# Performance work log

Hardware: AMD Instinct MI355X
Metric: run time of the kernel (lower is better)

Reference implementation:

```python
import jax, jax.numpy as jnp
import numpy as np

N_NODES = 16384
N_EDGES = 131072
N_GRAPHS = 16
U_SZ, U_RED = 4096, 256
EDGE_H, EDGE_OUT = 1024, 512
NODE_H = 512
NODE_IN = 9  # 4 + 5, hard-coded in OGRENet
EDGE_IN = 1


def _lin_init(k, fan_in, fan_out):
    k1, k2 = jax.random.split(k)
    bound = 1.0 / np.sqrt(fan_in)
    W = jax.random.uniform(k1, (fan_in, fan_out), jnp.float32, -bound, bound)
    b = jax.random.uniform(k2, (fan_out,), jnp.float32, -bound, bound)
    return W, b


def setup_inputs() -> dict:
    key = jax.random.key(0)
    ks = jax.random.split(key, 16)
    inp = {
        "x": jax.random.normal(ks[0], (N_NODES, NODE_IN), jnp.float32),
        "edge_attr": jax.random.normal(ks[1], (N_EDGES, EDGE_IN), jnp.float32),
        "u": jax.random.normal(ks[2], (N_GRAPHS, U_SZ), jnp.float32),
        "edge_index": jax.random.randint(ks[3], (2, N_EDGES), 0, N_NODES, jnp.int64 if jax.config.jax_enable_x64 else jnp.int32).astype(jnp.int32),
        "batch": jnp.sort(jax.random.randint(ks[4], (N_NODES,), 0, N_GRAPHS)).astype(jnp.int32),
    }
    # global dim reduction 4096 -> 256
    inp["w_dr"], inp["b_dr"] = _lin_init(ks[5], U_SZ, U_RED)
    # edge MLP: in = 1 + 2*9 + 256 = 275
    e_in = EDGE_IN + 2 * NODE_IN + U_RED
    inp["e_w0"], inp["e_b0"] = _lin_init(ks[6], e_in, EDGE_H)
    inp["e_w1"], inp["e_b1"] = _lin_init(ks[7], EDGE_H, EDGE_H)
    inp["e_w2"], inp["e_b2"] = _lin_init(ks[8], EDGE_H, EDGE_H)
    inp["e_w3"], inp["e_b3"] = _lin_init(ks[9], EDGE_H, EDGE_H)
    inp["e_wf"], inp["e_bf"] = _lin_init(ks[10], EDGE_H, EDGE_OUT)
    # node mlp 1: in = 9 + 512 = 521
    inp["n1_w0"], inp["n1_b0"] = _lin_init(ks[11], NODE_IN + EDGE_OUT, NODE_H)
    inp["n1_w1"], inp["n1_b1"] = _lin_init(ks[12], NODE_H, NODE_H)
    # node mlp 2: in = 9 + 512 + 256 = 777, out = 1
    inp["n2_w0"], inp["n2_b0"] = _lin_init(ks[13], NODE_IN + NODE_H + U_RED, NODE_H)
    inp["n2_w1"], inp["n2_b1"] = _lin_init(ks[14], NODE_H, 1)
    return inp


def reference(x, edge_attr, u, edge_index, batch,
              w_dr, b_dr,
              e_w0, e_b0, e_w1, e_b1, e_w2, e_b2, e_w3, e_b3, e_wf, e_bf,
              n1_w0, n1_b0, n1_w1, n1_b1,
              n2_w0, n2_b0, n2_w1, n2_b1):
    relu = jax.nn.relu
    # select_dim_reduction
    u_r = u @ w_dr + b_dr  # [G, 256]
    row, col = edge_index[0], edge_index[1]
    # EdgeModel: cat([src, dest, edge_attr, u[batch[row]]])
    e_in = jnp.concatenate([x[row], x[col], edge_attr, u_r[batch[row]]], axis=1)
    h = relu(e_in @ e_w0 + e_b0)
    h = relu(h @ e_w1 + e_b1)
    h = relu(h @ e_w2 + e_b2)
    h = relu(h @ e_w3 + e_b3)
    e = h @ e_wf + e_bf  # [E, 512]
    # NodeModel: mlp1 on cat([x[col], edge_attr_new]) then scatter_mean by row
    n_in = jnp.concatenate([x[col], e], axis=1)
    h = relu(n_in @ n1_w0 + n1_b0)
    h = relu(h @ n1_w1 + n1_b1)  # [E, 512]
    agg = jax.ops.segment_sum(h, row, num_segments=N_NODES)
    cnt = jax.ops.segment_sum(jnp.ones((h.shape[0],), h.dtype), row, num_segments=N_NODES)
    agg = agg / jnp.maximum(cnt, 1.0)[:, None]  # scatter_mean (zeros stay zero)
    o = jnp.concatenate([x, agg, u_r[batch]], axis=1)
    o = relu(o @ n2_w0 + n2_b0) @ n2_w1 + n2_b1  # [N, 1]
    return jnp.squeeze(o, axis=-1)
```

## Files before the change

kernel.cpp:

```cpp
#include <hip/hip_runtime.h>
#include <type_traits>
#include <utility>
#include <cstdint>

typedef unsigned short u16;
typedef __attribute__((ext_vector_type(4))) float f32x4;
typedef __attribute__((ext_vector_type(8))) short s16x8;
typedef __attribute__((ext_vector_type(8))) __bf16 b16x8;

template <typename T, typename = void> struct MfmaTakes : std::false_type {};
template <typename T>
struct MfmaTakes<T, std::void_t<decltype(__builtin_amdgcn_mfma_f32_16x16x32_bf16(
    std::declval<T>(), std::declval<T>(), std::declval<f32x4>(), 0, 0, 0))>>
    : std::true_type {};
using abvec = std::conditional_t<MfmaTakes<s16x8>::value, s16x8, b16x8>;
static_assert(sizeof(abvec) == 16, "frag must be 4 VGPRs");

template <typename T>
__device__ __forceinline__ f32x4 mfma_bf16(T a, T b, f32x4 c) {
  return __builtin_amdgcn_mfma_f32_16x16x32_bf16(a, b, c, 0, 0, 0);
}

__device__ __forceinline__ float b2f(u16 v) {
  union { unsigned u; float f; } x; x.u = ((unsigned)v) << 16; return x.f;
}
__device__ __forceinline__ u16 f2b(float f) {
  union { float f; unsigned u; } x; x.f = f;
  unsigned r = x.u + 0x7fffu + ((x.u >> 16) & 1u);
  return (u16)(r >> 16);
}

__device__ __forceinline__ void gld16(const void* g, void* l) {
  auto gp = reinterpret_cast<const __attribute__((address_space(1))) unsigned int*>(
      reinterpret_cast<uintptr_t>(g));
  auto lp = reinterpret_cast<__attribute__((address_space(3))) unsigned int*>(
      reinterpret_cast<uintptr_t>(l));
  __builtin_amdgcn_global_load_lds(gp, lp, 16, 0, 0);
}

#define NN 16384
#define NE 131072
#define NG 16

__global__ void detect_dtype(const u16* __restrict__ x, int* __restrict__ flag) {
  __shared__ int cnt;
  if (threadIdx.x == 0) cnt = 0;
  __syncthreads();
  int local = 0;
#pragma unroll
  for (int i = 0; i < 8; i++) {
    u16 h = x[threadIdx.x * 8 + i];
    int e = (h >> 7) & 0xFF;
    if (h == 0 || (e >= 110 && e <= 134)) local++;
  }
  atomicAdd(&cnt, local);
  __syncthreads();
  if (threadIdx.x == 0) *flag = (cnt >= 1700) ? 1 : 0;
}

struct CvtJob {
  const void* src[14];
  void* dst[14];
  int n[14];
};

__global__ __launch_bounds__(256) void cvt_all(CvtJob jb, const int* __restrict__ flag) {
  const int idx = blockIdx.x * 256 + threadIdx.x;
  const int f = *flag;
  int off = 0;
#pragma unroll
  for (int j = 0; j < 14; j++) {
    const int nn = jb.n[j];
    if (idx < off + nn) {
      const int i = idx - off;
      u16 v = f ? ((const u16*)jb.src[j])[i]
                : f2b(((const float*)jb.src[j])[i]);
      ((u16*)jb.dst[j])[i] = v;
      return;
    }
    off += nn;
  }
}

__global__ __launch_bounds__(256) void cvt_plain(
    const void* __restrict__ src, u16* __restrict__ dst, int n,
    const int* __restrict__ flag)
{
  const int i = blockIdx.x * 256 + threadIdx.x;
  if (i >= n) return;
  dst[i] = *flag ? ((const u16*)src)[i] : f2b(((const float*)src)[i]);
}

__global__ __launch_bounds__(256, 3) void gemm_bt(
    const u16* __restrict__ A, const u16* __restrict__ Bt,
    const u16* __restrict__ bias, u16* __restrict__ C,
    int M, int N, int K, int ldc, int relu)
{
  __shared__ alignas(16) u16 smem[24576];
  const int tid = threadIdx.x;
  const int wave = tid >> 6, lane = tid & 63;
  const int m0 = blockIdx.x * 128, n0 = blockIdx.y * 128;

  const int srow = lane >> 2;
  const int kslot = lane & 3;
  const int sswz = (srow >> 1) & 3;
  const u16* gA = A + (size_t)(m0 + wave * 32 + srow) * K + (kslot ^ sswz) * 8;
  const u16* gB = Bt + (size_t)(n0 + wave * 32 + srow) * K + (kslot ^ sswz) * 8;
  const int loff = (wave * 32 + srow) * 32 + kslot * 8;

  const int wm = (wave >> 1) * 64;
  const int wn = (wave & 1) * 64;
  const int fr = lane & 15;
  const int fks = ((lane >> 4) ^ ((fr >> 1) & 3)) * 8;

  f32x4 acc[4][4] = {};
  const int NT = K >> 5;

#define STAGE(t, s) do { \
    const int o_ = (t) * 32; \
    u16* S_ = smem + (s) * 8192; \
    gld16(gA + o_, S_ + loff); gld16(gA + 16 * (size_t)K + o_, S_ + loff + 512); \
    gld16(gB + o_, S_ + 4096 + loff); gld16(gB + 16 * (size_t)K + o_, S_ + 4096 + loff + 512); \
  } while (0)

  STAGE(0, 0);
  if (NT > 1) {
    STAGE(1, 1);
    __asm__ volatile("s_waitcnt vmcnt(4)" ::: "memory");
  } else {
    __asm__ volatile("s_waitcnt vmcnt(0)" ::: "memory");
  }
  __builtin_amdgcn_s_barrier();

  int sl = 0;
  for (int t = 0; t < NT; t++) {
    if (t + 2 < NT) {
      const int sw = (sl + 2 >= 3) ? sl - 1 : sl + 2;
      STAGE(t + 2, sw);
    }
    const u16* As = smem + sl * 8192;
    const u16* Bs = As + 4096;
    abvec af[4], bf[4];
#pragma unroll
    for (int i = 0; i < 4; i++)
      af[i] = *(const abvec*)&As[(wm + i * 16 + fr) * 32 + fks];
#pragma unroll
    for (int i = 0; i < 4; i++)
      bf[i] = *(const abvec*)&Bs[(wn + i * 16 + fr) * 32 + fks];
    __builtin_amdgcn_s_setprio(1);
#pragma unroll
    for (int mi = 0; mi < 4; mi++)
#pragma unroll
      for (int ni = 0; ni < 4; ni++)
        acc[mi][ni] = mfma_bf16(af[mi], bf[ni], acc[mi][ni]);
    __builtin_amdgcn_s_setprio(0);
    if (t + 2 < NT) __asm__ volatile("s_waitcnt vmcnt(4)" ::: "memory");
    else            __asm__ volatile("s_waitcnt vmcnt(0)" ::: "memory");
    __builtin_amdgcn_s_barrier();
    sl = (sl == 2) ? 0 : sl + 1;
  }
#undef STAGE

  const int crow0 = (lane >> 4) * 4;
  float bv[4];
#pragma unroll
  for (int ni = 0; ni < 4; ni++) bv[ni] = b2f(bias[n0 + wn + ni * 16 + fr]);

  u16* W = smem + wave * 4096;
#pragma unroll
  for (int mi = 0; mi < 4; mi++) {
#pragma unroll
    for (int ni = 0; ni < 4; ni++) {
      f32x4 v = acc[mi][ni];
      const int colx = ni * 16 + fr;
      const int cl = colx & 7, ch = colx >> 3;
#pragma unroll
      for (int r = 0; r < 4; r++) {
        const int rowx = mi * 16 + crow0 + r;
        float f = v[r] + bv[ni];
        if (relu) f = fmaxf(f, 0.0f);
        W[rowx * 64 + ((ch ^ (rowx & 7)) << 3) + cl] = f2b(f);
      }
    }
  }
  __asm__ volatile("s_waitcnt lgkmcnt(0)" ::: "memory");
#pragma unroll
  for (int p = 0; p < 8; p++) {
    const int rowx = p * 8 + (lane >> 3);
    const int pc = lane & 7;
    const int lc = pc ^ (rowx & 7);
    s16x8 val = *(const s16x8*)&W[rowx * 64 + pc * 8];
    *(s16x8*)&C[(size_t)(m0 + wm + rowx) * ldc + n0 + wn + lc * 8] = val;
  }
}

__global__ __launch_bounds__(1024) void gemm256b(
    const u16* __restrict__ A, const u16* __restrict__ Bt,
    const u16* __restrict__ bias, u16* __restrict__ C,
    int K, int ldc, int relu)
{
  __shared__ alignas(16) u16 smem[49152];
  const int tid = threadIdx.x;
  const int wave = tid >> 6, lane = tid & 63;
  const int wr = wave >> 2, wc = wave & 3;
  const int m0 = blockIdx.x << 8, n0 = blockIdx.y << 8;

  const int srow = tid >> 2;
  const int kslot = tid & 3;
  const int sswz = (srow >> 1) & 3;
  const u16* gA = A  + (size_t)(m0 + srow) * K + (kslot ^ sswz) * 8;
  const u16* gB = Bt + (size_t)(n0 + srow) * K + (kslot ^ sswz) * 8;
  const int loff = tid * 8;

  const int fr = lane & 15;
  const int fks = ((lane >> 4) ^ ((fr >> 1) & 3)) * 8;
  const int aob = (wr * 64 + fr) * 32 + fks;
  const int bob = (wc * 64 + fr) * 32 + fks;

  f32x4 acc[4][4] = {};
  const int NT = K >> 5;

#define STAGE2(t, s) do { \
    const int o_ = (t) * 32; \
    u16* S_ = smem + (s) * 16384; \
    gld16(gA + o_, S_ + loff); gld16(gB + o_, S_ + 8192 + loff); \
  } while (0)

  STAGE2(0, 0);
  if (NT > 1) {
    STAGE2(1, 1);
    __asm__ volatile("s_waitcnt vmcnt(2)" ::: "memory");
  } else {
    __asm__ volatile("s_waitcnt vmcnt(0)" ::: "memory");
  }
  __builtin_amdgcn_s_barrier();

  int sl = 0;
  for (int t = 0; t < NT; t++) {
    if (t + 2 < NT) {
      const int sw = (sl + 2 >= 3) ? sl - 1 : sl + 2;
      STAGE2(t + 2, sw);
    }
    const u16* As = smem + sl * 16384;
    const u16* Bs = As + 8192;
    abvec af[4], bf[4];
#pragma unroll
    for (int i = 0; i < 4; i++)
      af[i] = *(const abvec*)&As[aob + i * 512];
#pragma unroll
    for (int i = 0; i < 4; i++)
      bf[i] = *(const abvec*)&Bs[bob + i * 512];
    __builtin_amdgcn_s_setprio(1);
#pragma unroll
    for (int mi = 0; mi < 4; mi++)
#pragma unroll
      for (int ni = 0; ni < 4; ni++)
        acc[mi][ni] = mfma_bf16(af[mi], bf[ni], acc[mi][ni]);
    __builtin_amdgcn_s_setprio(0);
    if (t + 2 < NT) __asm__ volatile("s_waitcnt vmcnt(2)" ::: "memory");
    else            __asm__ volatile("s_waitcnt vmcnt(0)" ::: "memory");
    __builtin_amdgcn_s_barrier();
    sl = (sl == 2) ? 0 : sl + 1;
  }
#undef STAGE2

  const int crow0 = (lane >> 4) * 4;
  float bv[4];
#pragma unroll
  for (int ni = 0; ni < 4; ni++) bv[ni] = b2f(bias[n0 + wc * 64 + ni * 16 + fr]);
  u16* W = smem + wave * 2048;
#pragma unroll
  for (int h = 0; h < 2; h++) {
    if (h) __asm__ volatile("s_waitcnt lgkmcnt(0)" ::: "memory");
#pragma unroll
    for (int mi = 0; mi < 4; mi++) {
#pragma unroll
      for (int nh = 0; nh < 2; nh++) {
        const int ni = h * 2 + nh;
        f32x4 v = acc[mi][ni];
        const int colx = nh * 16 + fr;
        const int cl = colx & 7, ch = colx >> 3;
#pragma unroll
        for (int r = 0; r < 4; r++) {
          const int rowx = mi * 16 + crow0 + r;
          float f = v[r] + bv[ni];
          if (relu) f = fmaxf(f, 0.0f);
          W[rowx * 32 + ((ch ^ (rowx & 3)) << 3) + cl] = f2b(f);
        }
      }
    }
    __asm__ volatile("s_waitcnt lgkmcnt(0)" ::: "memory");
#pragma unroll
    for (int p = 0; p < 4; p++) {
      const int rowx = p * 16 + (lane >> 2);
      const int pc = lane & 3;
      const int lc = pc ^ (rowx & 3);
      s16x8 val = *(const s16x8*)&W[rowx * 32 + pc * 8];
      *(s16x8*)&C[(size_t)(m0 + wr * 64 + rowx) * ldc + n0 + wc * 64 + h * 32 + lc * 8] = val;
    }
  }
}

__global__ __launch_bounds__(256) void transpose_pad(
    const void* __restrict__ src, u16* __restrict__ dst, int K, int N, int Kp,
    int perm, int k0, const int* __restrict__ flag)
{
  __shared__ u16 tile[32][33];
  const int f = *flag;
  const u16* s16p = (const u16*)src;
  const float* sfp = (const float*)src;
  const int kb = blockIdx.x * 32, nb = blockIdx.y * 32;
  const int tx = threadIdx.x & 31, ty = threadIdx.x >> 5;
#pragma unroll
  for (int i = 0; i < 32; i += 8) {
    int k = kb + ty + i, n = nb + tx;
    u16 v = 0;
    if (k < K && n < N)
      v = f ? s16p[(size_t)(k0 + k) * N + n] : f2b(sfp[(size_t)(k0 + k) * N + n]);
    tile[ty + i][tx] = v;
  }
  __syncthreads();
#pragma unroll
  for (int i = 0; i < 32; i += 8) {
    int n = nb + ty + i, k = kb + tx;
    if (n < N && k < Kp) {
      int nk = perm ? (k < 9 ? 512 + k : (k < 521 ? k - 9 : k)) : k;
      dst[(size_t)n * Kp + nk] = tile[tx][ty + i];
    }
  }
}

__global__ __launch_bounds__(256) void fuse_tail(
    const u16* __restrict__ n1w0t, u16* __restrict__ fused)
{
  const int idx = blockIdx.x * 256 + threadIdx.x;
  const int p = idx >> 5, t = idx & 31;
  fused[p * 1056 + 1024 + t] = n1w0t[p * 544 + 512 + t];
}

__global__ __launch_bounds__(256) void fuse_bias(
    const u16* __restrict__ ebf, const u16* __restrict__ n1b0,
    const u16* __restrict__ n1w0e, u16* __restrict__ fb)
{
  const int p = blockIdx.x * 256 + threadIdx.x;
  float acc = b2f(n1b0[p]);
#pragma unroll 8
  for (int j = 0; j < 512; j++) acc += b2f(ebf[j]) * b2f(n1w0e[p * 512 + j]);
  fb[p] = f2b(acc);
}

__global__ __launch_bounds__(256) void dim_reduce2(
    const u16* __restrict__ u, const void* __restrict__ w,
    float* __restrict__ uacc, const int* __restrict__ flag)
{
  const int g = blockIdx.x, kt = blockIdx.y, j = threadIdx.x;
  const int f = *flag;
  __shared__ u16 us[512];
  us[j] = u[g * 4096 + kt * 512 + j];
  us[256 + j] = u[g * 4096 + kt * 512 + 256 + j];
  __syncthreads();
  float acc = 0.0f;
  if (f) {
    const u16* wp = (const u16*)w + (size_t)(kt * 512) * 256 + j;
#pragma unroll 8
    for (int k = 0; k < 512; k++) acc += b2f(us[k]) * b2f(wp[(size_t)k * 256]);
  } else {
    const float* wp = (const float*)w + (size_t)(kt * 512) * 256 + j;
#pragma unroll 8
    for (int k = 0; k < 512; k++) acc += b2f(us[k]) * wp[(size_t)k * 256];
  }
  atomicAdd(&uacc[g * 256 + j], acc);
}

__global__ __launch_bounds__(256) void finish_ur(
    const float* __restrict__ uacc, const u16* __restrict__ bdr,
    u16* __restrict__ ur)
{
  const int i = blockIdx.x * 256 + threadIdx.x;
  ur[i] = f2b(uacc[i] + b2f(bdr[i & 255]));
}

__global__ __launch_bounds__(256) void count_edges(
    const int* __restrict__ row, int* __restrict__ cnt)
{
  const int e = blockIdx.x * 256 + threadIdx.x;
  if (e < NE) atomicAdd(&cnt[row[e]], 1);
}

__global__ __launch_bounds__(256) void prefix_offs(
    const int* __restrict__ cnt, int* __restrict__ offs, int* __restrict__ cursor)
{
  __shared__ int part[256];
  __shared__ int base[256];
  const int t = threadIdx.x;
  int s = 0;
#pragma unroll
  for (int i = 0; i < 64; i++) s += cnt[t * 64 + i];
  part[t] = s;
  __syncthreads();
  if (t == 0) {
    int r = 0;
    for (int i = 0; i < 256; i++) { base[i] = r; r += part[i]; }
  }
  __syncthreads();
  int r = base[t];
#pragma unroll
  for (int i = 0; i < 64; i++) {
    const int n = t * 64 + i;
    offs[n] = r; cursor[n] = r; r += cnt[n];
  }
  if (t == 255) offs[16384] = r;
}

__global__ __launch_bounds__(256) void build_perm(
    const int* __restrict__ row, int* __restrict__ cursor, int* __restrict__ eperm)
{
  const int e = blockIdx.x * 256 + threadIdx.x;
  const int pos = atomicAdd(&cursor[row[e]], 1);
  eperm[pos] = e;
}

__global__ __launch_bounds__(256) void build_ein(
    const u16* __restrict__ x, const u16* __restrict__ ea,
    const u16* __restrict__ ur, const int* __restrict__ row,
    const int* __restrict__ col, const int* __restrict__ batch,
    const int* __restrict__ eperm, u16* __restrict__ out, int e0)
{
  const int idx = blockIdx.x * 256 + threadIdx.x;
  const int le = idx / 40, g = idx % 40;
  const int c0 = g * 8;
  const int e = eperm[e0 + le];
  const int r = row[e];
  alignas(16) u16 v[8];
  if (c0 >= 24 && c0 + 8 <= 275) {
    const u16* up = &ur[batch[r] * 256 + (c0 - 19)];
#pragma unroll
    for (int j = 0; j < 8; j++) v[j] = up[j];
  } else {
    const int cl = col[e];
    const int b = batch[r];
#pragma unroll
    for (int j = 0; j < 8; j++) {
      const int c = c0 + j;
      u16 t;
      if (c < 9)        t = x[r * 9 + c];
      else if (c < 18)  t = x[cl * 9 + (c - 9)];
      else if (c == 18) t = ea[e];
      else if (c < 275) t = ur[b * 256 + (c - 19)];
      else              t = 0;
      v[j] = t;
    }
  }
  *(s16x8*)&out[(size_t)le * 320 + c0] = *(const s16x8*)v;
}

__global__ __launch_bounds__(256) void fill_h_tail(
    const u16* __restrict__ x, const int* __restrict__ col,
    const int* __restrict__ eperm, u16* __restrict__ out, int e0)
{
  const int idx = blockIdx.x * 256 + threadIdx.x;
  const int le = idx >> 2, j8 = idx & 3;
  const int c0 = 1024 + j8 * 8;
  const int cl = col[eperm[e0 + le]];
  alignas(16) u16 v[8];
#pragma unroll
  for (int j = 0; j < 8; j++) {
    const int c = c0 + j;
    v[j] = (c < 1033) ? x[cl * 9 + (c - 1024)] : (u16)0;
  }
  *(s16x8*)&out[(size_t)le * 1056 + c0] = *(const s16x8*)v;
}

__global__ __launch_bounds__(256) void seg_reduce(
    const u16* __restrict__ h, const int* __restrict__ offs,
    float* __restrict__ agg, int e0, int echunk)
{
  const int wave = threadIdx.x >> 6, lane = threadIdx.x & 63;
  const int n = blockIdx.x * 4 + wave;
  int lo = offs[n], hi = offs[n + 1];
  const int first = (lo >= e0);
  lo = lo > e0 ? lo : e0;
  const int e1 = e0 + echunk;
  hi = hi < e1 ? hi : e1;
  if (lo >= hi) return;
  const int c0 = lane * 8;
  float acc[8] = {};
  for (int i = lo; i < hi; i++) {
    s16x8 v = *(const s16x8*)&h[(size_t)(i - e0) * 512 + c0];
#pragma unroll
    for (int j = 0; j < 8; j++) acc[j] += b2f((u16)v[j]);
  }
  float* ap = &agg[(size_t)n * 512 + c0];
  if (first) {
#pragma unroll
    for (int j = 0; j < 8; j++) ap[j] = acc[j];
  } else {
#pragma unroll
    for (int j = 0; j < 8; j++) ap[j] += acc[j];
  }
}

__global__ __launch_bounds__(256) void build_nin2(
    const u16* __restrict__ x, const float* __restrict__ agg,
    const int* __restrict__ cnt, const u16* __restrict__ ur,
    const int* __restrict__ batch, u16* __restrict__ out, int n0)
{
  const int idx = blockIdx.x * 256 + threadIdx.x;
  const int le = idx / 100, g = idx % 100;
  const int c0 = g * 8;
  const int n = n0 + le;
  alignas(16) u16 v[8];
  if (c0 < 512) {
    const int cn = cnt[n];
    if (cn == 0) {
#pragma unroll
      for (int j = 0; j < 8; j++) v[j] = 0;
    } else {
      const float den = (float)cn;
      const f32x4* ap = (const f32x4*)&agg[(size_t)n * 512 + c0];
      f32x4 a0 = ap[0], a1 = ap[1];
#pragma unroll
      for (int j = 0; j < 4; j++) { v[j] = f2b(a0[j] / den); v[4 + j] = f2b(a1[j] / den); }
    }
  } else {
    const int b = batch[n];
#pragma unroll
    for (int j = 0; j < 8; j++) {
      const int c = c0 + j;
      u16 t;
      if (c < 521)      t = x[n * 9 + (c - 512)];
      else if (c < 777) t = ur[b * 256 + (c - 521)];
      else              t = 0;
      v[j] = t;
    }
  }
  *(s16x8*)&out[(size_t)le * 800 + c0] = *(const s16x8*)v;
}

__global__ __launch_bounds__(256) void final_dot(
    const u16* __restrict__ h, const u16* __restrict__ w,
    const u16* __restrict__ b, void* __restrict__ out, int n0,
    const int* __restrict__ flag)
{
  const int wave = threadIdx.x >> 6, lane = threadIdx.x & 63;
  const int n = blockIdx.x * 4 + wave;
  const u16* hp = h + (size_t)n * 512 + lane * 8;
  const u16* wp = w + lane * 8;
  float s = 0.0f;
#pragma unroll
  for (int i = 0; i < 8; i++) s += b2f(hp[i]) * b2f(wp[i]);
#pragma unroll
  for (int off = 32; off > 0; off >>= 1) s += __shfl_down(s, off, 64);
  if (lane == 0) {
    float r = s + b2f(b[0]);
    if (*flag) ((u16*)out)[n0 + n] = f2b(r);
    else       ((float*)out)[n0 + n] = r;
  }
}

constexpr size_t OFF_FLAG = 0;
constexpr size_t OFF_XC   = 64;
constexpr size_t OFF_EAC  = OFF_XC   + 147456ull * 2;
constexpr size_t OFF_UC   = OFF_EAC  + 131072ull * 2;
constexpr size_t OFF_BDR  = OFF_UC   + 65536ull * 2;
constexpr size_t OFF_EB0  = OFF_BDR  + 256ull * 2;
constexpr size_t OFF_EB1  = OFF_EB0  + 1024ull * 2;
constexpr size_t OFF_EB2  = OFF_EB1  + 1024ull * 2;
constexpr size_t OFF_EB3  = OFF_EB2  + 1024ull * 2;
constexpr size_t OFF_EBF  = OFF_EB3  + 1024ull * 2;
constexpr size_t OFF_N1B0 = OFF_EBF  + 512ull * 2;
constexpr size_t OFF_N1B1 = OFF_N1B0 + 512ull * 2;
constexpr size_t OFF_N2B0 = OFF_N1B1 + 512ull * 2;
constexpr size_t OFF_N2W1 = OFF_N2B0 + 512ull * 2;
constexpr size_t OFF_N2B1 = OFF_N2W1 + 512ull * 2;
constexpr size_t OFF_OFFS = (OFF_N2B1 + 64 + 63) & ~63ull;
constexpr size_t OFF_CUR  = OFF_OFFS + 16388ull * 4;
constexpr size_t OFF_UACC = OFF_CUR  + 16384ull * 4;
static_assert(OFF_UACC + 4096 * 4 < (1ull << 20), "params+small fit in 1MB");

constexpr size_t OFF_W0T  = 1ull << 20;
constexpr size_t OFF_W1T  = OFF_W0T  + 1024ull * 320 * 2;
constexpr size_t OFF_W2T  = OFF_W1T  + 1024ull * 1024 * 2;
constexpr size_t OFF_W3T  = OFF_W2T  + 1024ull * 1024 * 2;
constexpr size_t OFF_WFC  = OFF_W3T  + 1024ull * 1024 * 2;
constexpr size_t OFF_N1W0 = OFF_WFC  + 1024ull * 512 * 2;
constexpr size_t OFF_N1W1 = OFF_N1W0 + 512ull * 544 * 2;
constexpr size_t OFF_N2W0 = OFF_N1W1 + 512ull * 512 * 2;
constexpr size_t OFF_N1WE = OFF_N2W0 + 512ull * 800 * 2;
constexpr size_t OFF_FUSE = OFF_N1WE + 512ull * 512 * 2;
constexpr size_t OFF_FB   = OFF_FUSE + 512ull * 1056 * 2;
constexpr size_t OFF_ZB   = OFF_FB   + 512ull * 2;
constexpr size_t OFF_UR   = OFF_ZB   + 1024ull * 2;
constexpr size_t OFF_CNT  = OFF_UR   + 16ull * 256 * 2;
constexpr size_t OFF_AGG  = OFF_CNT  + 16384ull * 4;
constexpr size_t OFF_BUF0 = OFF_AGG  + 16384ull * 512 * 4;

extern "C" void kernel_launch(void* const* d_in, const int* in_sizes, int n_in,
                              void* d_out, int out_size, void* d_ws, size_t ws_size,
                              hipStream_t stream) {
  const void* x_r  = d_in[0];
  const void* ea_r = d_in[1];
  const void* u_r  = d_in[2];
  const int*  ei    = (const int*)d_in[3];
  const int*  batch = (const int*)d_in[4];
  const void* w_dr = d_in[5];
  const void* b_dr = d_in[6];
  const void* e_w0 = d_in[7];  const void* e_b0 = d_in[8];
  const void* e_w1 = d_in[9];  const void* e_b1 = d_in[10];
  const void* e_w2 = d_in[11]; const void* e_b2 = d_in[12];
  const void* e_w3 = d_in[13]; const void* e_b3 = d_in[14];
  const void* e_wf = d_in[15]; const void* e_bf = d_in[16];
  const void* n1w0 = d_in[17]; const void* n1b0 = d_in[18];
  const void* n1w1 = d_in[19]; const void* n1b1 = d_in[20];
  const void* n2w0 = d_in[21]; const void* n2b0 = d_in[22];
  const void* n2w1 = d_in[23]; const void* n2b1 = d_in[24];

  const int* row = ei;
  const int* col = ei + NE;

  char* ws = (char*)d_ws;
  int*   FLAG = (int*)(ws + OFF_FLAG);
  u16*   XC   = (u16*)(ws + OFF_XC);
  u16*   EAC  = (u16*)(ws + OFF_EAC);
  u16*   UC   = (u16*)(ws + OFF_UC);
  u16*   BDRC = (u16*)(ws + OFF_BDR);
  u16*   EB0C = (u16*)(ws + OFF_EB0);
  u16*   EB1C = (u16*)(ws + OFF_EB1);
  u16*   EB2C = (u16*)(ws + OFF_EB2);
  u16*   EB3C = (u16*)(ws + OFF_EB3);
  u16*   EBFC = (u16*)(ws + OFF_EBF);
  u16*   N1B0C= (u16*)(ws + OFF_N1B0);
  u16*   N1B1C= (u16*)(ws + OFF_N1B1);
  u16*   N2B0C= (u16*)(ws + OFF_N2B0);
  u16*   N2W1C= (u16*)(ws + OFF_N2W1);
  u16*   N2B1C= (u16*)(ws + OFF_N2B1);
  int*   OFFS = (int*)(ws + OFF_OFFS);
  int*   CUR  = (int*)(ws + OFF_CUR);
  float* UACC = (float*)(ws + OFF_UACC);
  u16*   W0T  = (u16*)(ws + OFF_W0T);
  u16*   W1T  = (u16*)(ws + OFF_W1T);
  u16*   W2T  = (u16*)(ws + OFF_W2T);
  u16*   W3T  = (u16*)(ws + OFF_W3T);
  u16*   WFC  = (u16*)(ws + OFF_WFC);
  u16*   N1W0T= (u16*)(ws + OFF_N1W0);
  u16*   N1W1T= (u16*)(ws + OFF_N1W1);
  u16*   N2W0T= (u16*)(ws + OFF_N2W0);
  u16*   N1WE = (u16*)(ws + OFF_N1WE);
  u16*   FUSED= (u16*)(ws + OFF_FUSE);
  u16*   FB   = (u16*)(ws + OFF_FB);
  u16*   ZB   = (u16*)(ws + OFF_ZB);
  u16*   UR   = (u16*)(ws + OFF_UR);
  int*   CNT  = (int*)(ws + OFF_CNT);
  float* AGG  = (float*)(ws + OFF_AGG);
  (void)in_sizes; (void)n_in; (void)out_size;

  int echunk = 16384;
  while (echunk > 2048 &&
         OFF_BUF0 + (size_t)echunk * 4224 + (size_t)NE * 4 > ws_size) echunk >>= 1;
  u16* P    = (u16*)(ws + OFF_BUF0);
  u16* Q    = (u16*)(ws + OFF_BUF0 + (size_t)echunk * 2112);
  int* EPRM = (int*)(ws + OFF_BUF0 + (size_t)echunk * 4224);
  const int nchunks = NE / echunk;
  const int nodch = echunk < NN ? echunk : NN;
  const int nodchn = NN / nodch;

  detect_dtype<<<1, 256, 0, stream>>>((const u16*)x_r, FLAG);

  CvtJob jb;
  const void* srcs[14] = {x_r, ea_r, u_r, b_dr, e_b0, e_b1, e_b2, e_b3,
                          e_bf, n1b0, n1b1, n2b0, n2w1, n2b1};
  void* dsts[14] = {XC, EAC, UC, BDRC, EB0C, EB1C, EB2C, EB3C,
                    EBFC, N1B0C, N1B1C, N2B0C, N2W1C, N2B1C};
  const int ns[14] = {147456, 131072, 65536, 256, 1024, 1024, 1024, 1024,
                      512, 512, 512, 512, 512, 1};
  int tot = 0;
  for (int j = 0; j < 14; j++) { jb.src[j] = srcs[j]; jb.dst[j] = dsts[j]; jb.n[j] = ns[j]; tot += ns[j]; }
  cvt_all<<<(tot + 255) / 256, 256, 0, stream>>>(jb, FLAG);

  transpose_pad<<<dim3(10, 32), 256, 0, stream>>>(e_w0, W0T,  275, 1024, 320, 0, 0, FLAG);
  transpose_pad<<<dim3(32, 32), 256, 0, stream>>>(e_w1, W1T, 1024, 1024, 1024, 0, 0, FLAG);
  transpose_pad<<<dim3(32, 32), 256, 0, stream>>>(e_w2, W2T, 1024, 1024, 1024, 0, 0, FLAG);
  transpose_pad<<<dim3(32, 32), 256, 0, stream>>>(e_w3, W3T, 1024, 1024, 1024, 0, 0, FLAG);
  transpose_pad<<<dim3(17, 16), 256, 0, stream>>>(n1w0, N1W0T, 521, 512, 544, 1, 0, FLAG);
  transpose_pad<<<dim3(16, 16), 256, 0, stream>>>(n1w1, N1W1T, 512, 512, 512, 0, 0, FLAG);
  transpose_pad<<<dim3(25, 16), 256, 0, stream>>>(n2w0, N2W0T, 777, 512, 800, 1, 0, FLAG);
  transpose_pad<<<dim3(16, 16), 256, 0, stream>>>(n1w0, N1WE, 512, 512, 512, 0, 9, FLAG);
  cvt_plain<<<2048, 256, 0, stream>>>(e_wf, WFC, 1024 * 512, FLAG);

  (void)hipMemsetAsync(UACC, 0, 4096ull * 4, stream);
  (void)hipMemsetAsync(CNT, 0, 16384ull * 4, stream);
  (void)hipMemsetAsync(ZB, 0, 2048, stream);

  gemm_bt<<<dim3(4, 8), 256, 0, stream>>>(N1WE, WFC, ZB, FUSED, 512, 1024, 512, 1056, 0);
  fuse_tail<<<64, 256, 0, stream>>>(N1W0T, FUSED);
  fuse_bias<<<2, 256, 0, stream>>>(EBFC, N1B0C, N1WE, FB);

  dim_reduce2<<<dim3(NG, 8), 256, 0, stream>>>(UC, w_dr, UACC, FLAG);
  finish_ur<<<16, 256, 0, stream>>>(UACC, BDRC, UR);

  count_edges<<<NE / 256, 256, 0, stream>>>(row, CNT);
  prefix_offs<<<1, 256, 0, stream>>>(CNT, OFFS, CUR);
  build_perm<<<NE / 256, 256, 0, stream>>>(row, CUR, EPRM);

  for (int c = 0; c < nchunks; c++) {
    const int e0 = c * echunk;
    build_ein<<<echunk * 40 / 256, 256, 0, stream>>>(XC, EAC, UR, row, col, batch, EPRM, P, e0);
    gemm256b<<<dim3(echunk / 256, 4), 1024, 0, stream>>>(P, W0T, EB0C, Q, 320, 1024, 1);
    gemm256b<<<dim3(echunk / 256, 4), 1024, 0, stream>>>(Q, W1T, EB1C, P, 1024, 1024, 1);
    gemm256b<<<dim3(echunk / 256, 4), 1024, 0, stream>>>(P, W2T, EB2C, Q, 1024, 1024, 1);
    gemm256b<<<dim3(echunk / 256, 4), 1024, 0, stream>>>(Q, W3T, EB3C, P, 1024, 1056, 1);
    fill_h_tail<<<echunk * 4 / 256, 256, 0, stream>>>(XC, col, EPRM, P, e0);
    gemm_bt<<<dim3(echunk / 128, 4), 256, 0, stream>>>(P, FUSED, FB, Q, echunk, 512, 1056, 512, 1);
    gemm_bt<<<dim3(echunk / 128, 4), 256, 0, stream>>>(Q, N1W1T, N1B1C, P, echunk, 512, 512, 512, 1);
    seg_reduce<<<NN / 4, 256, 0, stream>>>(P, OFFS, AGG, e0, echunk);
  }

  for (int c = 0; c < nodchn; c++) {
    const int n0 = c * nodch;
    build_nin2<<<nodch * 100 / 256, 256, 0, stream>>>(XC, AGG, CNT, UR, batch, P, n0);
    gemm_bt<<<dim3(nodch / 128, 4), 256, 0, stream>>>(P, N2W0T, N2B0C, Q, nodch, 512, 800, 512, 1);
    final_dot<<<nodch / 4, 256, 0, stream>>>(Q, N2W1C, N2B1C, d_out, n0, FLAG);
  }
}
```

Before: 1.755 ms.

## Precompute per-graph u_r projections and add them as per-row bias in GEMMs

The u_r part of the edge MLP's first layer and of node MLP2's first layer depends only on the graph, so a 16-row table of u_r@W (plus bias) is precomputed. The GEMMs now add a gathered per-row bias from that table through an index array. This shrinks K from 320 to 32 for the first edge layer and from 800 to 544 for the node layer, and cuts the input-build traffic. The cost is an extra gathered load per output element in the epilogue and slight rounding differences from the precomputed bf16 bias.

```diff
diff --git a/kernel.cpp b/kernel.cpp
--- a/kernel.cpp
+++ b/kernel.cpp
@@ -94,7 +94,8 @@
 __global__ __launch_bounds__(256, 3) void gemm_bt(
     const u16* __restrict__ A, const u16* __restrict__ Bt,
     const u16* __restrict__ bias, u16* __restrict__ C,
-    int M, int N, int K, int ldc, int relu)
+    int M, int N, int K, int ldc, int relu,
+    const u16* __restrict__ rb, const int* __restrict__ ridx, int rbs)
 {
   __shared__ alignas(16) u16 smem[24576];
   const int tid = threadIdx.x;
@@ -178,6 +179,7 @@
       for (int r = 0; r < 4; r++) {
         const int rowx = mi * 16 + crow0 + r;
         float f = v[r] + bv[ni];
+        if (rb) f += b2f(rb[(size_t)ridx[m0 + wm + rowx] * rbs + n0 + wn + ni * 16 + fr]);
         if (relu) f = fmaxf(f, 0.0f);
         W[rowx * 64 + ((ch ^ (rowx & 7)) << 3) + cl] = f2b(f);
       }
@@ -197,7 +199,8 @@
 __global__ __launch_bounds__(1024) void gemm256b(
     const u16* __restrict__ A, const u16* __restrict__ Bt,
     const u16* __restrict__ bias, u16* __restrict__ C,
-    int K, int ldc, int relu)
+    int K, int ldc, int relu,
+    const u16* __restrict__ rb, const int* __restrict__ ridx, int rbs)
 {
   __shared__ alignas(16) u16 smem[49152];
   const int tid = threadIdx.x;
@@ -284,6 +287,7 @@
         for (int r = 0; r < 4; r++) {
           const int rowx = mi * 16 + crow0 + r;
           float f = v[r] + bv[ni];
+          if (rb) f += b2f(rb[(size_t)ridx[m0 + wr * 64 + rowx] * rbs + n0 + wc * 64 + ni * 16 + fr]);
           if (relu) f = fmaxf(f, 0.0f);
           W[rowx * 32 + ((ch ^ (rowx & 3)) << 3) + cl] = f2b(f);
         }
@@ -347,6 +351,54 @@
 #pragma unroll 8
   for (int j = 0; j < 512; j++) acc += b2f(ebf[j]) * b2f(n1w0e[p * 512 + j]);
   fb[p] = f2b(acc);
+}
+
+__global__ __launch_bounds__(256) void make_uwb(
+    const void* __restrict__ w0, const u16* __restrict__ ur,
+    const u16* __restrict__ eb0, u16* __restrict__ uwb,
+    const int* __restrict__ flag)
+{
+  const int g = blockIdx.x;
+  const int n = blockIdx.y * 256 + threadIdx.x;
+  const int f = *flag;
+  __shared__ u16 us[256];
+  us[threadIdx.x] = ur[g * 256 + threadIdx.x];
+  __syncthreads();
+  float acc = b2f(eb0[n]);
+  if (f) {
+    const u16* wp = (const u16*)w0 + 19ull * 1024 + n;
+#pragma unroll 8
+    for (int j = 0; j < 256; j++) acc += b2f(us[j]) * b2f(wp[(size_t)j * 1024]);
+  } else {
+    const float* wp = (const float*)w0 + 19ull * 1024 + n;
+#pragma unroll 8
+    for (int j = 0; j < 256; j++) acc += b2f(us[j]) * wp[(size_t)j * 1024];
+  }
+  uwb[g * 1024 + n] = f2b(acc);
+}
+
+__global__ __launch_bounds__(256) void make_uw2(
+    const void* __restrict__ w, const u16* __restrict__ ur,
+    const u16* __restrict__ b0, u16* __restrict__ uw2,
+    const int* __restrict__ flag)
+{
+  const int g = blockIdx.x;
+  const int p = blockIdx.y * 256 + threadIdx.x;
+  const int f = *flag;
+  __shared__ u16 us[256];
+  us[threadIdx.x] = ur[g * 256 + threadIdx.x];
+  __syncthreads();
+  float acc = b2f(b0[p]);
+  if (f) {
+    const u16* wp = (const u16*)w + 521ull * 512 + p;
+#pragma unroll 8
+    for (int j = 0; j < 256; j++) acc += b2f(us[j]) * b2f(wp[(size_t)j * 512]);
+  } else {
+    const float* wp = (const float*)w + 521ull * 512 + p;
+#pragma unroll 8
+    for (int j = 0; j < 256; j++) acc += b2f(us[j]) * wp[(size_t)j * 512];
+  }
+  uw2[g * 512 + p] = f2b(acc);
 }
 
 __global__ __launch_bounds__(256) void dim_reduce2(
@@ -420,38 +472,31 @@
   eperm[pos] = e;
 }
 
-__global__ __launch_bounds__(256) void build_ein(
+__global__ __launch_bounds__(256) void build_ein2(
     const u16* __restrict__ x, const u16* __restrict__ ea,
-    const u16* __restrict__ ur, const int* __restrict__ row,
-    const int* __restrict__ col, const int* __restrict__ batch,
-    const int* __restrict__ eperm, u16* __restrict__ out, int e0)
+    const int* __restrict__ row, const int* __restrict__ col,
+    const int* __restrict__ batch, const int* __restrict__ eperm,
+    u16* __restrict__ out, int* __restrict__ bidx, int e0)
 {
   const int idx = blockIdx.x * 256 + threadIdx.x;
-  const int le = idx / 40, g = idx % 40;
+  const int le = idx >> 2, g = idx & 3;
   const int c0 = g * 8;
   const int e = eperm[e0 + le];
   const int r = row[e];
+  const int cl = col[e];
+  if (g == 0) bidx[le] = batch[r];
   alignas(16) u16 v[8];
-  if (c0 >= 24 && c0 + 8 <= 275) {
-    const u16* up = &ur[batch[r] * 256 + (c0 - 19)];
-#pragma unroll
-    for (int j = 0; j < 8; j++) v[j] = up[j];
-  } else {
-    const int cl = col[e];
-    const int b = batch[r];
-#pragma unroll
-    for (int j = 0; j < 8; j++) {
-      const int c = c0 + j;
-      u16 t;
-      if (c < 9)        t = x[r * 9 + c];
-      else if (c < 18)  t = x[cl * 9 + (c - 9)];
-      else if (c == 18) t = ea[e];
-      else if (c < 275) t = ur[b * 256 + (c - 19)];
-      else              t = 0;
-      v[j] = t;
-    }
-  }
-  *(s16x8*)&out[(size_t)le * 320 + c0] = *(const s16x8*)v;
+#pragma unroll
+  for (int j = 0; j < 8; j++) {
+    const int c = c0 + j;
+    u16 t;
+    if (c < 9)        t = x[r * 9 + c];
+    else if (c < 18)  t = x[cl * 9 + (c - 9)];
+    else if (c == 18) t = ea[e];
+    else              t = 0;
+    v[j] = t;
+  }
+  *(s16x8*)&out[(size_t)le * 32 + c0] = *(const s16x8*)v;
 }
 
 __global__ __launch_bounds__(256) void fill_h_tail(
@@ -502,11 +547,10 @@
 
 __global__ __launch_bounds__(256) void build_nin2(
     const u16* __restrict__ x, const float* __restrict__ agg,
-    const int* __restrict__ cnt, const u16* __restrict__ ur,
-    const int* __restrict__ batch, u16* __restrict__ out, int n0)
+    const int* __restrict__ cnt, u16* __restrict__ out, int n0)
 {
   const int idx = blockIdx.x * 256 + threadIdx.x;
-  const int le = idx / 100, g = idx % 100;
+  const int le = idx / 68, g = idx % 68;
   const int c0 = g * 8;
   const int n = n0 + le;
   alignas(16) u16 v[8];
@@ -523,18 +567,13 @@
       for (int j = 0; j < 4; j++) { v[j] = f2b(a0[j] / den); v[4 + j] = f2b(a1[j] / den); }
     }
   } else {
-    const int b = batch[n];
 #pragma unroll
     for (int j = 0; j < 8; j++) {
       const int c = c0 + j;
-      u16 t;
-      if (c < 521)      t = x[n * 9 + (c - 512)];
-      else if (c < 777) t = ur[b * 256 + (c - 521)];
-      else              t = 0;
-      v[j] = t;
-    }
-  }
-  *(s16x8*)&out[(size_t)le * 800 + c0] = *(const s16x8*)v;
+      v[j] = (c < 521) ? x[n * 9 + (c - 512)] : (u16)0;
+    }
+  }
+  *(s16x8*)&out[(size_t)le * 544 + c0] = *(const s16x8*)v;
 }
 
 __global__ __launch_bounds__(256) void final_dot(
@@ -590,7 +629,9 @@
 constexpr size_t OFF_FUSE = OFF_N1WE + 512ull * 512 * 2;
 constexpr size_t OFF_FB   = OFF_FUSE + 512ull * 1056 * 2;
 constexpr size_t OFF_ZB   = OFF_FB   + 512ull * 2;
-constexpr size_t OFF_UR   = OFF_ZB   + 1024ull * 2;
+constexpr size_t OFF_UWB  = OFF_ZB   + 1024ull * 2;
+constexpr size_t OFF_UW2  = OFF_UWB  + 16384ull * 2;
+constexpr size_t OFF_UR   = OFF_UW2  + 8192ull * 2;
 constexpr size_t OFF_CNT  = OFF_UR   + 16ull * 256 * 2;
 constexpr size_t OFF_AGG  = OFF_CNT  + 16384ull * 4;
 constexpr size_t OFF_BUF0 = OFF_AGG  + 16384ull * 512 * 4;
@@ -649,6 +690,8 @@
   u16*   FUSED= (u16*)(ws + OFF_FUSE);
   u16*   FB   = (u16*)(ws + OFF_FB);
   u16*   ZB   = (u16*)(ws + OFF_ZB);
+  u16*   UWB  = (u16*)(ws + OFF_UWB);
+  u16*   UW2  = (u16*)(ws + OFF_UW2);
   u16*   UR   = (u16*)(ws + OFF_UR);
   int*   CNT  = (int*)(ws + OFF_CNT);
   float* AGG  = (float*)(ws + OFF_AGG);
@@ -656,10 +699,11 @@
 
   int echunk = 16384;
   while (echunk > 2048 &&
-         OFF_BUF0 + (size_t)echunk * 4224 + (size_t)NE * 4 > ws_size) echunk >>= 1;
+         OFF_BUF0 + (size_t)echunk * 4228 + (size_t)NE * 4 > ws_size) echunk >>= 1;
   u16* P    = (u16*)(ws + OFF_BUF0);
   u16* Q    = (u16*)(ws + OFF_BUF0 + (size_t)echunk * 2112);
   int* EPRM = (int*)(ws + OFF_BUF0 + (size_t)echunk * 4224);
+  int* BIDX = EPRM + NE;
   const int nchunks = NE / echunk;
   const int nodch = echunk < NN ? echunk : NN;
   const int nodchn = NN / nodch;
@@ -677,13 +721,13 @@
   for (int j = 0; j < 14; j++) { jb.src[j] = srcs[j]; jb.dst[j] = dsts[j]; jb.n[j] = ns[j]; tot += ns[j]; }
   cvt_all<<<(tot + 255) / 256, 256, 0, stream>>>(jb, FLAG);
 
-  transpose_pad<<<dim3(10, 32), 256, 0, stream>>>(e_w0, W0T,  275, 1024, 320, 0, 0, FLAG);
+  transpose_pad<<<dim3(1, 32),  256, 0, stream>>>(e_w0, W0T,   19, 1024, 32, 0, 0, FLAG);
   transpose_pad<<<dim3(32, 32), 256, 0, stream>>>(e_w1, W1T, 1024, 1024, 1024, 0, 0, FLAG);
   transpose_pad<<<dim3(32, 32), 256, 0, stream>>>(e_w2, W2T, 1024, 1024, 1024, 0, 0, FLAG);
   transpose_pad<<<dim3(32, 32), 256, 0, stream>>>(e_w3, W3T, 1024, 1024, 1024, 0, 0, FLAG);
   transpose_pad<<<dim3(17, 16), 256, 0, stream>>>(n1w0, N1W0T, 521, 512, 544, 1, 0, FLAG);
   transpose_pad<<<dim3(16, 16), 256, 0, stream>>>(n1w1, N1W1T, 512, 512, 512, 0, 0, FLAG);
-  transpose_pad<<<dim3(25, 16), 256, 0, stream>>>(n2w0, N2W0T, 777, 512, 800, 1, 0, FLAG);
+  transpose_pad<<<dim3(17, 16), 256, 0, stream>>>(n2w0, N2W0T, 521, 512, 544, 1, 0, FLAG);
   transpose_pad<<<dim3(16, 16), 256, 0, stream>>>(n1w0, N1WE, 512, 512, 512, 0, 9, FLAG);
   cvt_plain<<<2048, 256, 0, stream>>>(e_wf, WFC, 1024 * 512, FLAG);
 
@@ -691,12 +735,15 @@
   (void)hipMemsetAsync(CNT, 0, 16384ull * 4, stream);
   (void)hipMemsetAsync(ZB, 0, 2048, stream);
 
-  gemm_bt<<<dim3(4, 8), 256, 0, stream>>>(N1WE, WFC, ZB, FUSED, 512, 1024, 512, 1056, 0);
+  gemm_bt<<<dim3(4, 8), 256, 0, stream>>>(N1WE, WFC, ZB, FUSED, 512, 1024, 512, 1056, 0,
+                                          nullptr, nullptr, 0);
   fuse_tail<<<64, 256, 0, stream>>>(N1W0T, FUSED);
   fuse_bias<<<2, 256, 0, stream>>>(EBFC, N1B0C, N1WE, FB);
 
   dim_reduce2<<<dim3(NG, 8), 256, 0, stream>>>(UC, w_dr, UACC, FLAG);
   finish_ur<<<16, 256, 0, stream>>>(UACC, BDRC, UR);
+  make_uwb<<<dim3(16, 4), 256, 0, stream>>>(e_w0, UR, EB0C, UWB, FLAG);
+  make_uw2<<<dim3(16, 2), 256, 0, stream>>>(n2w0, UR, N2B0C, UW2, FLAG);
 
   count_edges<<<NE / 256, 256, 0, stream>>>(row, CNT);
   prefix_offs<<<1, 256, 0, stream>>>(CNT, OFFS, CUR);
@@ -704,21 +751,28 @@
 
   for (int c = 0; c < nchunks; c++) {
     const int e0 = c * echunk;
-    build_ein<<<echunk * 40 / 256, 256, 0, stream>>>(XC, EAC, UR, row, col, batch, EPRM, P, e0);
-    gemm256b<<<dim3(echunk / 256, 4), 1024, 0, stream>>>(P, W0T, EB0C, Q, 320, 1024, 1);
-    gemm256b<<<dim3(echunk / 256, 4), 1024, 0, stream>>>(Q, W1T, EB1C, P, 1024, 1024, 1);
-    gemm256b<<<dim3(echunk / 256, 4), 1024, 0, stream>>>(P, W2T, EB2C, Q, 1024, 1024, 1);
-    gemm256b<<<dim3(echunk / 256, 4), 1024, 0, stream>>>(Q, W3T, EB3C, P, 1024, 1056, 1);
+    build_ein2<<<echunk * 4 / 256, 256, 0, stream>>>(XC, EAC, row, col, batch, EPRM, P, BIDX, e0);
+    gemm256b<<<dim3(echunk / 256, 4), 1024, 0, stream>>>(P, W0T, ZB, Q, 32, 1024, 1,
+                                                         UWB, BIDX, 1024);
+    gemm256b<<<dim3(echunk / 256, 4), 1024, 0, stream>>>(Q, W1T, EB1C, P, 1024, 1024, 1,
+                                                         nullptr, nullptr, 0);
+    gemm256b<<<dim3(echunk / 256, 4), 1024, 0, stream>>>(P, W2T, EB2C, Q, 1024, 1024, 1,
+                                                         nullptr, nullptr, 0);
+    gemm256b<<<dim3(echunk / 256, 4), 1024, 0, stream>>>(Q, W3T, EB3C, P, 1024, 1056, 1,
+                                                         nullptr, nullptr, 0);
     fill_h_tail<<<echunk * 4 / 256, 256, 0, stream>>>(XC, col, EPRM, P, e0);
-    gemm_bt<<<dim3(echunk / 128, 4), 256, 0, stream>>>(P, FUSED, FB, Q, echunk, 512, 1056, 512, 1);
-    gemm_bt<<<dim3(echunk / 128, 4), 256, 0, stream>>>(Q, N1W1T, N1B1C, P, echunk, 512, 512, 512, 1);
+    gemm_bt<<<dim3(echunk / 128, 4), 256, 0, stream>>>(P, FUSED, FB, Q, echunk, 512, 1056, 512, 1,
+                                                       nullptr, nullptr, 0);
+    gemm_bt<<<dim3(echunk / 128, 4), 256, 0, stream>>>(Q, N1W1T, N1B1C, P, echunk, 512, 512, 512, 1,
+                                                       nullptr, nullptr, 0);
     seg_reduce<<<NN / 4, 256, 0, stream>>>(P, OFFS, AGG, e0, echunk);
   }
 
   for (int c = 0; c < nodchn; c++) {
     const int n0 = c * nodch;
-    build_nin2<<<nodch * 100 / 256, 256, 0, stream>>>(XC, AGG, CNT, UR, batch, P, n0);
-    gemm_bt<<<dim3(nodch / 128, 4), 256, 0, stream>>>(P, N2W0T, N2B0C, Q, nodch, 512, 800, 512, 1);
+    build_nin2<<<nodch * 68 / 256, 256, 0, stream>>>(XC, AGG, CNT, P, n0);
+    gemm_bt<<<dim3(nodch / 128, 4), 256, 0, stream>>>(P, N2W0T, ZB, Q, nodch, 512, 544, 512, 1,
+                                                      UW2, batch + n0, 512);
     final_dot<<<nodch / 4, 256, 0, stream>>>(Q, N2W1C, N2B1C, d_out, n0, FLAG);
   }
 }
```

Result: no change. 1.785 ms (+1.7%).
